# Optimization experiments

Measured on AMD Instinct MI355X. Metric: run time of the kernel, lower is better.

Reference implementation:

```python
import jax, jax.numpy as jnp
import numpy as np

CONNECTIONS = {0: [1, 7], 1: [0, 2], 2: [1, 3], 3: [2], 4: [0, 5], 5: [4, 6], 6: [5], 7: [0, 8], 8: [7, 9, 11, 14], 9: [8, 10], 10: [9], 11: [8, 12], 12: [11, 13], 13: [12], 14: [8, 15], 15: [14, 16], 16: [15]}
J = 17
DIM_IN = 128
DIM_OUT = 128
B, T = 64, 243


def _build_bases():
    A1 = np.zeros((J, J), dtype=np.float32)
    for i, neigh in CONNECTIONS.items():
        for j in neigh:
            A1[i, j] = 1.0
            A1[j, i] = 1.0
    eye = np.eye(J, dtype=np.float32)
    adj1_base = A1 + eye
    paths2 = (A1 @ A1 > 0).astype(np.float32)
    adj2_base = ((paths2 - A1 - eye) > 0).astype(np.float32)
    return jnp.asarray(adj1_base), jnp.asarray(adj2_base)


def setup_inputs() -> dict:
    key = jax.random.key(0)
    ks = jax.random.split(key, 8)
    adj1_base, adj2_base = _build_bases()
    # xavier_uniform with gain 1.414 for W
    bound_w = 1.414 * np.sqrt(6.0 / (DIM_IN + DIM_OUT))
    W = jax.random.uniform(ks[0], (DIM_IN, DIM_OUT), jnp.float32, -bound_w, bound_w)
    bound_b = 1.0 / np.sqrt(DIM_IN)
    b = jax.random.uniform(ks[1], (DIM_OUT,), jnp.float32, -bound_b, bound_b)
    return {
        "x": jax.random.normal(ks[2], (B, T, J, DIM_IN), jnp.float32),
        "W": W,
        "b": b,
        "adj_l1": jnp.zeros((J, J), jnp.float32),
        "adj_l2": jnp.zeros((J, J), jnp.float32),
        "w1": jnp.ones((1,), jnp.float32),
        "w2": jnp.ones((1,), jnp.float32),
        "gate_w": jax.random.normal(ks[3], (DIM_IN, 1), jnp.float32) / np.sqrt(DIM_IN),
        "gate_b": jnp.zeros((1,), jnp.float32),
        "bn_gamma": jnp.ones((DIM_OUT,), jnp.float32),
        "bn_beta": jnp.zeros((DIM_OUT,), jnp.float32),
        "adj1_base": adj1_base,
        "adj2_base": adj2_base,
    }


def reference(x, W, b, adj_l1, adj_l2, w1, w2, gate_w, gate_b, bn_gamma, bn_beta, adj1_base, adj2_base):
    Bb, Tt, Jj, C = x.shape
    xf = x.reshape(Bb * Tt, Jj, C)  # (N, J, C)

    # learnable-weighted static adjacency (symmetrized)
    A1w = adj1_base + jax.nn.sigmoid(adj_l1)
    A2w = adj2_base + jax.nn.sigmoid(adj_l2)
    comb = jax.nn.softplus(w1[0]) * A1w + jax.nn.softplus(w2[0]) * A2w
    comb = 0.5 * (comb + comb.T)  # (J, J)

    # dynamic cosine-similarity adjacency
    nrm = jnp.linalg.norm(xf, axis=-1, keepdims=True)
    xn = xf / jnp.maximum(nrm, 1e-12)
    dyn = jax.nn.relu(jnp.einsum("nic,njc->nij", xn, xn)) + jnp.eye(Jj, dtype=x.dtype)

    gate = jax.nn.sigmoid(xf @ gate_w + gate_b)  # (N, J, 1)
    A = gate * comb[None] + (1.0 - gate) * dyn  # (N, J, J)

    # symmetric degree normalization
    deg = A.sum(-1)  # (N, J)
    d = (deg + 1e-6) ** -0.5
    A_hat = d[:, :, None] * A * d[:, None, :]

    h = jnp.einsum("nij,njc->nic", A_hat, xf @ W) + b  # (N, J, dim_out)

    # BatchNorm1d over channels (training-mode batch stats over N and J)
    mean = h.mean(axis=(0, 1))
    var = h.var(axis=(0, 1))
    h = (h - mean) * jax.lax.rsqrt(var + 1e-5) * bn_gamma + bn_beta

    h = jax.nn.relu(h)
    h = h + xf  # residual (dim_in == dim_out -> identity projection)
    return h.reshape(Bb, Tt, Jj, -1)
```

## Files before the change

kernel.cpp:

```cpp
#include <hip/hip_runtime.h>

typedef unsigned short u16;
typedef unsigned int   u32;
typedef __attribute__((ext_vector_type(8))) short bfrag8;
typedef __attribute__((ext_vector_type(4))) float f32x4;

#define NSAMP  15552
#define GRID_B 3888
#define GRID_G 4131

__device__ __forceinline__ u32 bfr(float f){
  u32 u = __float_as_uint(f);
  return (u + 0x7FFFu + ((u >> 16) & 1u)) >> 16;
}
__device__ __forceinline__ u32 packbf(float lo, float hi){
  return bfr(lo) | (bfr(hi) << 16);
}
__device__ __forceinline__ float sigm(float v){ return 1.0f / (1.0f + __expf(-v)); }
__device__ __forceinline__ float softp(float v){ return (v > 20.f) ? v : log1pf(__expf(v)); }

__global__ void kA(const float* __restrict__ W, const float* __restrict__ al1,
                   const float* __restrict__ al2, const float* __restrict__ w1,
                   const float* __restrict__ w2, const float* __restrict__ a1b,
                   const float* __restrict__ a2b, u16* __restrict__ wt,
                   float* __restrict__ comb, float* __restrict__ mid){
  int idx = blockIdx.x * 256 + threadIdx.x;
  int k = idx >> 7, n = idx & 127;
  wt[n * 128 + k] = (u16)bfr(W[idx]);
  if (blockIdx.x == 1) mid[threadIdx.x] = 0.f;
  if (blockIdx.x == 0){
    float s1 = softp(w1[0]);
    float s2 = softp(w2[0]);
    for (int p = threadIdx.x; p < 289; p += 256){
      int i = p / 17, j = p - i * 17;
      float mij = s1 * (a1b[i*17+j] + sigm(al1[i*17+j])) + s2 * (a2b[i*17+j] + sigm(al2[i*17+j]));
      float mji = s1 * (a1b[j*17+i] + sigm(al1[j*17+i])) + s2 * (a2b[j*17+i] + sigm(al2[j*17+i]));
      comb[i*20 + j] = 0.5f * (mij + mji);
    }
  }
}

struct __align__(16) QSmem { u16 xb[4][18][136]; };
__global__ __launch_bounds__(256, 4) void kQ(const float* __restrict__ x,
    const float* __restrict__ gw, const float* __restrict__ gb,
    float* __restrict__ gbuf){
  __shared__ QSmem q;
  const int tid = threadIdx.x;
  const int w  = tid >> 6;
  const int l  = tid & 63;
  const int g4 = l >> 4;
  const int lc = l & 15;
  const int s  = blockIdx.x * 4 + w;
  const float* xs = x + (size_t)s * 2176;

  float2 g2 = *(const float2*)(gw + 2*l);
  *(u32*)&q.xb[w][17][2*l] = packbf(g2.x, g2.y);
  #pragma unroll
  for (int j = 0; j < 17; j++){
    float2 v = *(const float2*)(xs + j*128 + 2*l);
    *(u32*)&q.xb[w][j][2*l] = packbf(v.x, v.y);
  }
  __syncthreads();
  __builtin_amdgcn_sched_barrier(0);

  const int rB = 16 + ((lc < 2) ? lc : 1);
  f32x4 z4 = {0.f,0.f,0.f,0.f};
  f32x4 dg00 = z4, dg01 = z4, dg11 = z4;
  #pragma unroll
  for (int ks = 0; ks < 4; ks++){
    const int ko = ks*32 + (g4 << 3);
    bfrag8 a0 = *(const bfrag8*)&q.xb[w][lc][ko];
    bfrag8 a1 = *(const bfrag8*)&q.xb[w][rB][ko];
    dg00 = __builtin_amdgcn_mfma_f32_16x16x32_bf16(a0, a0, dg00, 0,0,0);
    dg01 = __builtin_amdgcn_mfma_f32_16x16x32_bf16(a0, a1, dg01, 0,0,0);
    dg11 = __builtin_amdgcn_mfma_f32_16x16x32_bf16(a1, a1, dg11, 0,0,0);
  }
  float* gs = gbuf + (size_t)s * 384;
  const float gbv = gb[0];
  #pragma unroll
  for (int r = 0; r < 4; r++){
    const int i = (g4 << 2) + r;
    gs[i*20 + lc] = dg00[r];
    if (lc == 0){ gs[i*20 + 16] = dg01[r]; gs[16*20 + i] = dg01[r]; }
    if (lc == 1){ gs[360 + i] = sigm(dg01[r] + gbv); }
  }
  if ((lc >> 2) == g4){
    float v = dg00[lc & 3];
    gs[340 + lc] = 1.0f / fmaxf(sqrtf(v), 1e-12f);
  }
  if (l == 0) gs[340 + 16] = 1.0f / fmaxf(sqrtf(dg11[0]), 1e-12f);
  if (l == 1) gs[360 + 16] = sigm(dg11[0] + gbv);
}

struct WaveMem {
  float G[17][20];
  float scr[64];
};
struct BSmem {
  WaveMem wm[4];
  float   combs[340];
};
static_assert(sizeof(BSmem) <= 81920, "LDS budget");

__global__ __launch_bounds__(256, 4) void kBl(
    const float* __restrict__ x, const float* __restrict__ combg,
    const float* __restrict__ gbuf, float* __restrict__ out){
  __shared__ BSmem sm;
  const int tid = threadIdx.x;
  const int w  = tid >> 6;
  const int l  = tid & 63;
  const int g4 = l >> 4;
  const int lc = l & 15;

  for (int p = tid; p < 340; p += 256) sm.combs[p] = combg[p];

  WaveMem& M = sm.wm[w];
  float* Mf = (float*)&M.G[0][0];
  const int s = blockIdx.x * 4 + w;
  const float* gs = gbuf + (size_t)s * 384;
  for (int p = l; p < 380; p += 64) Mf[p] = gs[p];

  const float* xs = x + (size_t)s * 2176;
  float2 xr[17];
  #pragma unroll
  for (int j = 0; j < 17; j++) xr[j] = *(const float2*)(xs + j*128 + 2*l);
  __syncthreads();

  const float iv16 = M.scr[16], gt16 = M.scr[36];
  const float ivj  = M.scr[lc];
  float av00[4], av01[4], dp0[4];
  #pragma unroll
  for (int r = 0; r < 4; r++){
    const int i0 = (g4 << 2) + r;
    const float iv0 = M.scr[i0], gi0 = M.scr[20 + i0];
    float dyn = (i0 == lc) ? 2.0f : fmaxf(M.G[i0][lc] * iv0 * ivj, 0.f);
    av00[r] = gi0 * sm.combs[i0*20 + lc] + (1.f - gi0) * dyn;
    float dyn16 = fmaxf(M.G[i0][16] * iv0 * iv16, 0.f);
    float a16 = gi0 * sm.combs[i0*20 + 16] + (1.f - gi0) * dyn16;
    av01[r] = (lc == 0) ? a16 : 0.f;
    dp0[r] = av00[r] + av01[r];
  }
  float dyn10 = fmaxf(M.G[16][lc] * iv16 * ivj, 0.f);
  float av10 = gt16 * sm.combs[16*20 + lc] + (1.f - gt16) * dyn10;
  float av11 = (lc == 0) ? (gt16 * sm.combs[16*20 + 16] + (1.f - gt16) * 2.0f) : 0.f;
  float dp1 = av10 + av11;
  #pragma unroll
  for (int m = 1; m <= 8; m <<= 1){
    #pragma unroll
    for (int r = 0; r < 4; r++) dp0[r] += __shfl_xor(dp0[r], m, 64);
    dp1 += __shfl_xor(dp1, m, 64);
  }
  float dd0[4];
  #pragma unroll
  for (int r = 0; r < 4; r++) dd0[r] = rsqrtf(dp0[r] + 1e-6f);
  float dd1 = rsqrtf(dp1 + 1e-6f);
  if (lc == 0){
    #pragma unroll
    for (int r = 0; r < 4; r++) M.scr[40 + (g4<<2) + r] = dd0[r];
  }
  if (l == 0) M.scr[40 + 16] = dd1;
  __syncthreads();

  const float dj0 = M.scr[40 + lc];
  const float dj1 = M.scr[40 + 16];
  #pragma unroll
  for (int r = 0; r < 4; r++){
    const int i0 = (g4 << 2) + r;
    M.G[i0][lc] = dd0[r] * av00[r] * dj0;
    if (lc == 0) M.G[i0][16] = dd0[r] * av01[r] * dj1;
  }
  if (g4 == 0) M.G[16][lc] = dd1 * av10 * dj0;
  if (l == 0)  M.G[16][16] = dd1 * av11 * dj1;
  __syncthreads();

  float* ob = out + (size_t)s * 2176;
  for (int i = 0; i < 17; i++){
    const float4 a0 = *(const float4*)&M.G[i][0];
    const float4 a1 = *(const float4*)&M.G[i][4];
    const float4 a2 = *(const float4*)&M.G[i][8];
    const float4 a3 = *(const float4*)&M.G[i][12];
    const float a16 = M.G[i][16];
    float zx = a0.x*xr[0].x,  zy = a0.x*xr[0].y;
    zx += a0.y*xr[1].x;  zy += a0.y*xr[1].y;
    zx += a0.z*xr[2].x;  zy += a0.z*xr[2].y;
    zx += a0.w*xr[3].x;  zy += a0.w*xr[3].y;
    zx += a1.x*xr[4].x;  zy += a1.x*xr[4].y;
    zx += a1.y*xr[5].x;  zy += a1.y*xr[5].y;
    zx += a1.z*xr[6].x;  zy += a1.z*xr[6].y;
    zx += a1.w*xr[7].x;  zy += a1.w*xr[7].y;
    zx += a2.x*xr[8].x;  zy += a2.x*xr[8].y;
    zx += a2.y*xr[9].x;  zy += a2.y*xr[9].y;
    zx += a2.z*xr[10].x; zy += a2.z*xr[10].y;
    zx += a2.w*xr[11].x; zy += a2.w*xr[11].y;
    zx += a3.x*xr[12].x; zy += a3.x*xr[12].y;
    zx += a3.y*xr[13].x; zy += a3.y*xr[13].y;
    zx += a3.z*xr[14].x; zy += a3.z*xr[14].y;
    zx += a3.w*xr[15].x; zy += a3.w*xr[15].y;
    zx += a16*xr[16].x;  zy += a16*xr[16].y;
    float2 zv; zv.x = zx; zv.y = zy;
    *(float2*)&ob[i*128 + 2*l] = zv;
  }
}

__global__ __launch_bounds__(256, 4) void kBf(
    const float* __restrict__ x, const float* __restrict__ gw,
    const float* __restrict__ gb, const float* __restrict__ combg,
    float* __restrict__ out){
  __shared__ BSmem sm;
  const int tid = threadIdx.x;
  const int w  = tid >> 6;
  const int l  = tid & 63;
  const int g4 = l >> 4;
  const int lc = l & 15;

  for (int p = tid; p < 340; p += 256) sm.combs[p] = combg[p];
  __syncthreads();

  WaveMem& M = sm.wm[w];
  float2 g2 = *(const float2*)(gw + 2*l);
  const float gbv = gb[0];
  const int s = blockIdx.x * 4 + w;
  const float* xs = x + (size_t)s * 2176;
  float2 xr[17];
  #pragma unroll
  for (int j = 0; j < 17; j++) xr[j] = *(const float2*)(xs + j*128 + 2*l);

  #pragma unroll
  for (int i = 0; i < 17; i++){
    float p[17];
    #pragma unroll
    for (int j = i; j < 17; j++)
      p[j-i] = xr[i].x*xr[j].x + xr[i].y*xr[j].y;
    float pg = xr[i].x*g2.x + xr[i].y*g2.y;
    #pragma unroll
    for (int m = 1; m <= 32; m <<= 1){
      #pragma unroll
      for (int j = i; j < 17; j++) p[j-i] += __shfl_xor(p[j-i], m, 64);
      pg += __shfl_xor(pg, m, 64);
    }
    #pragma unroll
    for (int j = i; j < 17; j++){
      if (l == j) M.G[i][j] = p[j-i];
      if (i != j && l == i) M.G[j][i] = p[j-i];
    }
    if (l == i){
      M.scr[i]      = 1.0f / fmaxf(sqrtf(p[0]), 1e-12f);
      M.scr[20 + i] = sigm(pg + gbv);
    }
  }
  __syncthreads();

  const float iv16 = M.scr[16], gt16 = M.scr[36];
  const float ivj  = M.scr[lc];
  float av00[4], av01[4], dp0[4];
  #pragma unroll
  for (int r = 0; r < 4; r++){
    const int i0 = (g4 << 2) + r;
    const float iv0 = M.scr[i0], gi0 = M.scr[20 + i0];
    float dyn = (i0 == lc) ? 2.0f : fmaxf(M.G[i0][lc] * iv0 * ivj, 0.f);
    av00[r] = gi0 * sm.combs[i0*20 + lc] + (1.f - gi0) * dyn;
    float dyn16 = fmaxf(M.G[i0][16] * iv0 * iv16, 0.f);
    float a16 = gi0 * sm.combs[i0*20 + 16] + (1.f - gi0) * dyn16;
    av01[r] = (lc == 0) ? a16 : 0.f;
    dp0[r] = av00[r] + av01[r];
  }
  float dyn10 = fmaxf(M.G[16][lc] * iv16 * ivj, 0.f);
  float av10 = gt16 * sm.combs[16*20 + lc] + (1.f - gt16) * dyn10;
  float av11 = (lc == 0) ? (gt16 * sm.combs[16*20 + 16] + (1.f - gt16) * 2.0f) : 0.f;
  float dp1 = av10 + av11;
  #pragma unroll
  for (int m = 1; m <= 8; m <<= 1){
    #pragma unroll
    for (int r = 0; r < 4; r++) dp0[r] += __shfl_xor(dp0[r], m, 64);
    dp1 += __shfl_xor(dp1, m, 64);
  }
  float dd0[4];
  #pragma unroll
  for (int r = 0; r < 4; r++) dd0[r] = rsqrtf(dp0[r] + 1e-6f);
  float dd1 = rsqrtf(dp1 + 1e-6f);
  if (lc == 0){
    #pragma unroll
    for (int r = 0; r < 4; r++) M.scr[40 + (g4<<2) + r] = dd0[r];
  }
  if (l == 0) M.scr[40 + 16] = dd1;
  __syncthreads();

  const float dj0 = M.scr[40 + lc];
  const float dj1 = M.scr[40 + 16];
  #pragma unroll
  for (int r = 0; r < 4; r++){
    const int i0 = (g4 << 2) + r;
    M.G[i0][lc] = dd0[r] * av00[r] * dj0;
    if (lc == 0) M.G[i0][16] = dd0[r] * av01[r] * dj1;
  }
  if (g4 == 0) M.G[16][lc] = dd1 * av10 * dj0;
  if (l == 0)  M.G[16][16] = dd1 * av11 * dj1;
  __syncthreads();

  float* ob = out + (size_t)s * 2176;
  for (int i = 0; i < 17; i++){
    const float4 a0 = *(const float4*)&M.G[i][0];
    const float4 a1 = *(const float4*)&M.G[i][4];
    const float4 a2 = *(const float4*)&M.G[i][8];
    const float4 a3 = *(const float4*)&M.G[i][12];
    const float a16 = M.G[i][16];
    float zx = a0.x*xr[0].x,  zy = a0.x*xr[0].y;
    zx += a0.y*xr[1].x;  zy += a0.y*xr[1].y;
    zx += a0.z*xr[2].x;  zy += a0.z*xr[2].y;
    zx += a0.w*xr[3].x;  zy += a0.w*xr[3].y;
    zx += a1.x*xr[4].x;  zy += a1.x*xr[4].y;
    zx += a1.y*xr[5].x;  zy += a1.y*xr[5].y;
    zx += a1.z*xr[6].x;  zy += a1.z*xr[6].y;
    zx += a1.w*xr[7].x;  zy += a1.w*xr[7].y;
    zx += a2.x*xr[8].x;  zy += a2.x*xr[8].y;
    zx += a2.y*xr[9].x;  zy += a2.y*xr[9].y;
    zx += a2.z*xr[10].x; zy += a2.z*xr[10].y;
    zx += a2.w*xr[11].x; zy += a2.w*xr[11].y;
    zx += a3.x*xr[12].x; zy += a3.x*xr[12].y;
    zx += a3.y*xr[13].x; zy += a3.y*xr[13].y;
    zx += a3.z*xr[14].x; zy += a3.z*xr[14].y;
    zx += a3.w*xr[15].x; zy += a3.w*xr[15].y;
    zx += a16*xr[16].x;  zy += a16*xr[16].y;
    float2 zv; zv.x = zx; zv.y = zy;
    *(float2*)&ob[i*128 + 2*l] = zv;
  }
}

struct __align__(16) GSmem {
  u16 wl[128][132];
  u16 zl[4][16][132];
};
__global__ __launch_bounds__(256, 3) void kG(const u16* __restrict__ wtg,
    float* __restrict__ mid, float* __restrict__ out){
  __shared__ GSmem g;
  const int tid = threadIdx.x;
  const int w  = tid >> 6;
  const int l  = tid & 63;
  const int g4 = l >> 4;
  const int lc = l & 15;

  for (int p = tid; p < 8192; p += 256){
    int n = p >> 6, k2 = (p & 63) * 2;
    *(u32*)&g.wl[n][k2] = ((const u32*)wtg)[p];
  }
  const int R = blockIdx.x * 64 + w * 16;
  float* zg = out + (size_t)R * 128;
  #pragma unroll
  for (int r = 0; r < 16; r++){
    float2 zv = *(const float2*)&zg[r*128 + 2*l];
    *(u32*)&g.zl[w][r][2*l] = packbf(zv.x, zv.y);
  }
  __syncthreads();
  __builtin_amdgcn_sched_barrier(0);

  f32x4 zero4 = {0.f,0.f,0.f,0.f};
  f32x4 acc[8];
  #pragma unroll
  for (int nf = 0; nf < 8; nf++) acc[nf] = zero4;
  #pragma unroll
  for (int ks = 0; ks < 4; ks++){
    const int ko = ks*32 + (g4 << 3);
    bfrag8 za = *(const bfrag8*)&g.zl[w][lc][ko];
    #pragma unroll
    for (int nf = 0; nf < 8; nf++){
      bfrag8 bw = *(const bfrag8*)&g.wl[nf*16 + lc][ko];
      acc[nf] = __builtin_amdgcn_mfma_f32_16x16x32_bf16(za, bw, acc[nf], 0,0,0);
    }
  }

  float s[8], q[8];
  #pragma unroll
  for (int nf = 0; nf < 8; nf++){
    float ss = 0.f, qq = 0.f;
    #pragma unroll
    for (int r = 0; r < 4; r++){
      float v = acc[nf][r];
      zg[(4*g4 + r)*128 + nf*16 + lc] = v;
      ss += v; qq += v*v;
    }
    ss += __shfl_xor(ss, 16, 64); ss += __shfl_xor(ss, 32, 64);
    qq += __shfl_xor(qq, 16, 64); qq += __shfl_xor(qq, 32, 64);
    s[nf] = ss; q[nf] = qq;
  }

  __syncthreads();
  float* stash = (float*)&g.zl[w][0][0];
  if (l < 16){
    #pragma unroll
    for (int nf = 0; nf < 8; nf++){
      stash[nf*16 + l]       = s[nf];
      stash[128 + nf*16 + l] = q[nf];
    }
  }
  __syncthreads();
  float t0 = ((float*)&g.zl[0][0][0])[tid];
  float t1 = ((float*)&g.zl[1][0][0])[tid];
  float t2 = ((float*)&g.zl[2][0][0])[tid];
  float t3 = ((float*)&g.zl[3][0][0])[tid];
  atomicAdd(&mid[tid], t0 + t1 + t2 + t3);
}

__global__ __launch_bounds__(256) void kD(const float* __restrict__ x,
    const float* __restrict__ mid, const float* __restrict__ gamma,
    const float* __restrict__ beta, float* __restrict__ out){
  __shared__ float sc[128], sh[128];
  const int t = threadIdx.x;
  if (t < 128){
    const float ic = 1.0f / 264384.0f;
    float mean = mid[t] * ic;
    float var  = fmaxf(mid[128 + t] * ic - mean*mean, 0.f);
    float scl  = gamma[t] * rsqrtf(var + 1e-5f);
    sc[t] = scl;
    sh[t] = beta[t] - mean * scl;
  }
  __syncthreads();
  const int total = 8460288;
  for (int i = blockIdx.x*256 + t; i < total; i += 2048*256){
    float4 h  = ((const float4*)out)[i];
    float4 xv = ((const float4*)x)[i];
    int c0 = (i & 31) << 2;
    float4 r;
    r.x = fmaxf(h.x*sc[c0+0] + sh[c0+0], 0.f) + xv.x;
    r.y = fmaxf(h.y*sc[c0+1] + sh[c0+1], 0.f) + xv.y;
    r.z = fmaxf(h.z*sc[c0+2] + sh[c0+2], 0.f) + xv.z;
    r.w = fmaxf(h.w*sc[c0+3] + sh[c0+3], 0.f) + xv.w;
    ((float4*)out)[i] = r;
  }
}

extern "C" void kernel_launch(void* const* d_in, const int* in_sizes, int n_in,
                              void* d_out, int out_size, void* d_ws, size_t ws_size,
                              hipStream_t stream){
  (void)in_sizes; (void)n_in; (void)out_size;
  const float* x     = (const float*)d_in[0];
  const float* W     = (const float*)d_in[1];
  const float* al1   = (const float*)d_in[3];
  const float* al2   = (const float*)d_in[4];
  const float* w1    = (const float*)d_in[5];
  const float* w2    = (const float*)d_in[6];
  const float* gw    = (const float*)d_in[7];
  const float* gb    = (const float*)d_in[8];
  const float* gamma = (const float*)d_in[9];
  const float* beta  = (const float*)d_in[10];
  const float* a1b   = (const float*)d_in[11];
  const float* a2b   = (const float*)d_in[12];
  float* out = (float*)d_out;

  float* wsf  = (float*)d_ws;
  float* comb = wsf;
  u16*   wt   = (u16*)(wsf + 384);
  float* mid  = wsf + 384 + 8192;
  float* gbuf = wsf + 384 + 8192 + 256;
  const size_t need = (size_t)(384 + 8192 + 256 + (size_t)NSAMP*384) * 4;

  hipLaunchKernelGGL(kA, dim3(64), dim3(256), 0, stream, W, al1, al2, w1, w2, a1b, a2b, wt, comb, mid);
  if (ws_size >= need){
    hipLaunchKernelGGL(kQ,  dim3(GRID_B), dim3(256), 0, stream, x, gw, gb, gbuf);
    hipLaunchKernelGGL(kBl, dim3(GRID_B), dim3(256), 0, stream, x, comb, gbuf, out);
  } else {
    hipLaunchKernelGGL(kBf, dim3(GRID_B), dim3(256), 0, stream, x, gw, gb, comb, out);
  }
  hipLaunchKernelGGL(kG, dim3(GRID_G), dim3(256), 0, stream, wt, mid, out);
  hipLaunchKernelGGL(kD, dim3(2048),   dim3(256), 0, stream, x, mid, gamma, beta, out);
}
```

Measured before the change: 256.3 us.

## Write aggregated features as bf16 to workspace and feed GEMM directly from global

The aggregation kernel now writes its A_hat·x result as packed bf16 into a separate workspace buffer instead of fp32 into the output. A new GEMM kernel reads these bf16 rows and the transposed weights straight from global memory into MFMA fragments, without staging them in LDS. It then writes h and accumulates per-channel batch-norm sums with atomics. The aim is to halve the intermediate traffic and drop the LDS staging and fp32-to-bf16 conversion in the GEMM. In exchange it needs a larger workspace and does more uncoalesced global reads of the weights.

```diff
diff --git a/kernel.cpp b/kernel.cpp
--- a/kernel.cpp
+++ b/kernel.cpp
@@ -102,9 +102,11 @@
 };
 static_assert(sizeof(BSmem) <= 81920, "LDS budget");
 
-__global__ __launch_bounds__(256, 4) void kBl(
+template<int ZOUT>
+__device__ __forceinline__ void kBl_body(
     const float* __restrict__ x, const float* __restrict__ combg,
-    const float* __restrict__ gbuf, float* __restrict__ out){
+    const float* __restrict__ gbuf, float* __restrict__ out,
+    u16* __restrict__ zbuf){
   __shared__ BSmem sm;
   const int tid = threadIdx.x;
   const int w  = tid >> 6;
@@ -124,6 +126,146 @@
   float2 xr[17];
   #pragma unroll
   for (int j = 0; j < 17; j++) xr[j] = *(const float2*)(xs + j*128 + 2*l);
+  __syncthreads();
+
+  const float iv16 = M.scr[16], gt16 = M.scr[36];
+  const float ivj  = M.scr[lc];
+  float av00[4], av01[4], dp0[4];
+  #pragma unroll
+  for (int r = 0; r < 4; r++){
+    const int i0 = (g4 << 2) + r;
+    const float iv0 = M.scr[i0], gi0 = M.scr[20 + i0];
+    float dyn = (i0 == lc) ? 2.0f : fmaxf(M.G[i0][lc] * iv0 * ivj, 0.f);
+    av00[r] = gi0 * sm.combs[i0*20 + lc] + (1.f - gi0) * dyn;
+    float dyn16 = fmaxf(M.G[i0][16] * iv0 * iv16, 0.f);
+    float a16 = gi0 * sm.combs[i0*20 + 16] + (1.f - gi0) * dyn16;
+    av01[r] = (lc == 0) ? a16 : 0.f;
+    dp0[r] = av00[r] + av01[r];
+  }
+  float dyn10 = fmaxf(M.G[16][lc] * iv16 * ivj, 0.f);
+  float av10 = gt16 * sm.combs[16*20 + lc] + (1.f - gt16) * dyn10;
+  float av11 = (lc == 0) ? (gt16 * sm.combs[16*20 + 16] + (1.f - gt16) * 2.0f) : 0.f;
+  float dp1 = av10 + av11;
+  #pragma unroll
+  for (int m = 1; m <= 8; m <<= 1){
+    #pragma unroll
+    for (int r = 0; r < 4; r++) dp0[r] += __shfl_xor(dp0[r], m, 64);
+    dp1 += __shfl_xor(dp1, m, 64);
+  }
+  float dd0[4];
+  #pragma unroll
+  for (int r = 0; r < 4; r++) dd0[r] = rsqrtf(dp0[r] + 1e-6f);
+  float dd1 = rsqrtf(dp1 + 1e-6f);
+  if (lc == 0){
+    #pragma unroll
+    for (int r = 0; r < 4; r++) M.scr[40 + (g4<<2) + r] = dd0[r];
+  }
+  if (l == 0) M.scr[40 + 16] = dd1;
+  __syncthreads();
+
+  const float dj0 = M.scr[40 + lc];
+  const float dj1 = M.scr[40 + 16];
+  #pragma unroll
+  for (int r = 0; r < 4; r++){
+    const int i0 = (g4 << 2) + r;
+    M.G[i0][lc] = dd0[r] * av00[r] * dj0;
+    if (lc == 0) M.G[i0][16] = dd0[r] * av01[r] * dj1;
+  }
+  if (g4 == 0) M.G[16][lc] = dd1 * av10 * dj0;
+  if (l == 0)  M.G[16][16] = dd1 * av11 * dj1;
+  __syncthreads();
+
+  float* ob = out + (size_t)s * 2176;
+  u16*   zb = zbuf + (size_t)s * 2176;
+  for (int i = 0; i < 17; i++){
+    const float4 a0 = *(const float4*)&M.G[i][0];
+    const float4 a1 = *(const float4*)&M.G[i][4];
+    const float4 a2 = *(const float4*)&M.G[i][8];
+    const float4 a3 = *(const float4*)&M.G[i][12];
+    const float a16 = M.G[i][16];
+    float zx = a0.x*xr[0].x,  zy = a0.x*xr[0].y;
+    zx += a0.y*xr[1].x;  zy += a0.y*xr[1].y;
+    zx += a0.z*xr[2].x;  zy += a0.z*xr[2].y;
+    zx += a0.w*xr[3].x;  zy += a0.w*xr[3].y;
+    zx += a1.x*xr[4].x;  zy += a1.x*xr[4].y;
+    zx += a1.y*xr[5].x;  zy += a1.y*xr[5].y;
+    zx += a1.z*xr[6].x;  zy += a1.z*xr[6].y;
+    zx += a1.w*xr[7].x;  zy += a1.w*xr[7].y;
+    zx += a2.x*xr[8].x;  zy += a2.x*xr[8].y;
+    zx += a2.y*xr[9].x;  zy += a2.y*xr[9].y;
+    zx += a2.z*xr[10].x; zy += a2.z*xr[10].y;
+    zx += a2.w*xr[11].x; zy += a2.w*xr[11].y;
+    zx += a3.x*xr[12].x; zy += a3.x*xr[12].y;
+    zx += a3.y*xr[13].x; zy += a3.y*xr[13].y;
+    zx += a3.z*xr[14].x; zy += a3.z*xr[14].y;
+    zx += a3.w*xr[15].x; zy += a3.w*xr[15].y;
+    zx += a16*xr[16].x;  zy += a16*xr[16].y;
+    if (ZOUT == 1){
+      *(u32*)&zb[i*128 + 2*l] = packbf(zx, zy);
+    } else {
+      float2 zv; zv.x = zx; zv.y = zy;
+      *(float2*)&ob[i*128 + 2*l] = zv;
+    }
+  }
+}
+
+__global__ __launch_bounds__(256, 4) void kBl2(
+    const float* __restrict__ x, const float* __restrict__ combg,
+    const float* __restrict__ gbuf, u16* __restrict__ zbuf){
+  kBl_body<1>(x, combg, gbuf, nullptr, zbuf);
+}
+__global__ __launch_bounds__(256, 4) void kBl(
+    const float* __restrict__ x, const float* __restrict__ combg,
+    const float* __restrict__ gbuf, float* __restrict__ out){
+  kBl_body<0>(x, combg, gbuf, out, nullptr);
+}
+
+__global__ __launch_bounds__(256, 4) void kBf(
+    const float* __restrict__ x, const float* __restrict__ gw,
+    const float* __restrict__ gb, const float* __restrict__ combg,
+    float* __restrict__ out){
+  __shared__ BSmem sm;
+  const int tid = threadIdx.x;
+  const int w  = tid >> 6;
+  const int l  = tid & 63;
+  const int g4 = l >> 4;
+  const int lc = l & 15;
+
+  for (int p = tid; p < 340; p += 256) sm.combs[p] = combg[p];
+  __syncthreads();
+
+  WaveMem& M = sm.wm[w];
+  float2 g2 = *(const float2*)(gw + 2*l);
+  const float gbv = gb[0];
+  const int s = blockIdx.x * 4 + w;
+  const float* xs = x + (size_t)s * 2176;
+  float2 xr[17];
+  #pragma unroll
+  for (int j = 0; j < 17; j++) xr[j] = *(const float2*)(xs + j*128 + 2*l);
+
+  #pragma unroll
+  for (int i = 0; i < 17; i++){
+    float p[17];
+    #pragma unroll
+    for (int j = i; j < 17; j++)
+      p[j-i] = xr[i].x*xr[j].x + xr[i].y*xr[j].y;
+    float pg = xr[i].x*g2.x + xr[i].y*g2.y;
+    #pragma unroll
+    for (int m = 1; m <= 32; m <<= 1){
+      #pragma unroll
+      for (int j = i; j < 17; j++) p[j-i] += __shfl_xor(p[j-i], m, 64);
+      pg += __shfl_xor(pg, m, 64);
+    }
+    #pragma unroll
+    for (int j = i; j < 17; j++){
+      if (l == j) M.G[i][j] = p[j-i];
+      if (i != j && l == i) M.G[j][i] = p[j-i];
+    }
+    if (l == i){
+      M.scr[i]      = 1.0f / fmaxf(sqrtf(p[0]), 1e-12f);
+      M.scr[20 + i] = sigm(pg + gbv);
+    }
+  }
   __syncthreads();
 
   const float iv16 = M.scr[16], gt16 = M.scr[36];
@@ -202,128 +344,57 @@
   }
 }
 
-__global__ __launch_bounds__(256, 4) void kBf(
-    const float* __restrict__ x, const float* __restrict__ gw,
-    const float* __restrict__ gb, const float* __restrict__ combg,
+__global__ __launch_bounds__(256, 4) void kG2(const u16* __restrict__ wtg,
+    const u16* __restrict__ zbuf, float* __restrict__ mid,
     float* __restrict__ out){
-  __shared__ BSmem sm;
+  __shared__ float stash[4][256];
   const int tid = threadIdx.x;
   const int w  = tid >> 6;
   const int l  = tid & 63;
   const int g4 = l >> 4;
   const int lc = l & 15;
-
-  for (int p = tid; p < 340; p += 256) sm.combs[p] = combg[p];
-  __syncthreads();
-
-  WaveMem& M = sm.wm[w];
-  float2 g2 = *(const float2*)(gw + 2*l);
-  const float gbv = gb[0];
-  const int s = blockIdx.x * 4 + w;
-  const float* xs = x + (size_t)s * 2176;
-  float2 xr[17];
-  #pragma unroll
-  for (int j = 0; j < 17; j++) xr[j] = *(const float2*)(xs + j*128 + 2*l);
-
-  #pragma unroll
-  for (int i = 0; i < 17; i++){
-    float p[17];
-    #pragma unroll
-    for (int j = i; j < 17; j++)
-      p[j-i] = xr[i].x*xr[j].x + xr[i].y*xr[j].y;
-    float pg = xr[i].x*g2.x + xr[i].y*g2.y;
-    #pragma unroll
-    for (int m = 1; m <= 32; m <<= 1){
-      #pragma unroll
-      for (int j = i; j < 17; j++) p[j-i] += __shfl_xor(p[j-i], m, 64);
-      pg += __shfl_xor(pg, m, 64);
-    }
-    #pragma unroll
-    for (int j = i; j < 17; j++){
-      if (l == j) M.G[i][j] = p[j-i];
-      if (i != j && l == i) M.G[j][i] = p[j-i];
-    }
-    if (l == i){
-      M.scr[i]      = 1.0f / fmaxf(sqrtf(p[0]), 1e-12f);
-      M.scr[20 + i] = sigm(pg + gbv);
-    }
-  }
-  __syncthreads();
-
-  const float iv16 = M.scr[16], gt16 = M.scr[36];
-  const float ivj  = M.scr[lc];
-  float av00[4], av01[4], dp0[4];
-  #pragma unroll
-  for (int r = 0; r < 4; r++){
-    const int i0 = (g4 << 2) + r;
-    const float iv0 = M.scr[i0], gi0 = M.scr[20 + i0];
-    float dyn = (i0 == lc) ? 2.0f : fmaxf(M.G[i0][lc] * iv0 * ivj, 0.f);
-    av00[r] = gi0 * sm.combs[i0*20 + lc] + (1.f - gi0) * dyn;
-    float dyn16 = fmaxf(M.G[i0][16] * iv0 * iv16, 0.f);
-    float a16 = gi0 * sm.combs[i0*20 + 16] + (1.f - gi0) * dyn16;
-    av01[r] = (lc == 0) ? a16 : 0.f;
-    dp0[r] = av00[r] + av01[r];
-  }
-  float dyn10 = fmaxf(M.G[16][lc] * iv16 * ivj, 0.f);
-  float av10 = gt16 * sm.combs[16*20 + lc] + (1.f - gt16) * dyn10;
-  float av11 = (lc == 0) ? (gt16 * sm.combs[16*20 + 16] + (1.f - gt16) * 2.0f) : 0.f;
-  float dp1 = av10 + av11;
-  #pragma unroll
-  for (int m = 1; m <= 8; m <<= 1){
-    #pragma unroll
-    for (int r = 0; r < 4; r++) dp0[r] += __shfl_xor(dp0[r], m, 64);
-    dp1 += __shfl_xor(dp1, m, 64);
-  }
-  float dd0[4];
-  #pragma unroll
-  for (int r = 0; r < 4; r++) dd0[r] = rsqrtf(dp0[r] + 1e-6f);
-  float dd1 = rsqrtf(dp1 + 1e-6f);
-  if (lc == 0){
-    #pragma unroll
-    for (int r = 0; r < 4; r++) M.scr[40 + (g4<<2) + r] = dd0[r];
-  }
-  if (l == 0) M.scr[40 + 16] = dd1;
-  __syncthreads();
-
-  const float dj0 = M.scr[40 + lc];
-  const float dj1 = M.scr[40 + 16];
-  #pragma unroll
-  for (int r = 0; r < 4; r++){
-    const int i0 = (g4 << 2) + r;
-    M.G[i0][lc] = dd0[r] * av00[r] * dj0;
-    if (lc == 0) M.G[i0][16] = dd0[r] * av01[r] * dj1;
-  }
-  if (g4 == 0) M.G[16][lc] = dd1 * av10 * dj0;
-  if (l == 0)  M.G[16][16] = dd1 * av11 * dj1;
-  __syncthreads();
-
-  float* ob = out + (size_t)s * 2176;
-  for (int i = 0; i < 17; i++){
-    const float4 a0 = *(const float4*)&M.G[i][0];
-    const float4 a1 = *(const float4*)&M.G[i][4];
-    const float4 a2 = *(const float4*)&M.G[i][8];
-    const float4 a3 = *(const float4*)&M.G[i][12];
-    const float a16 = M.G[i][16];
-    float zx = a0.x*xr[0].x,  zy = a0.x*xr[0].y;
-    zx += a0.y*xr[1].x;  zy += a0.y*xr[1].y;
-    zx += a0.z*xr[2].x;  zy += a0.z*xr[2].y;
-    zx += a0.w*xr[3].x;  zy += a0.w*xr[3].y;
-    zx += a1.x*xr[4].x;  zy += a1.x*xr[4].y;
-    zx += a1.y*xr[5].x;  zy += a1.y*xr[5].y;
-    zx += a1.z*xr[6].x;  zy += a1.z*xr[6].y;
-    zx += a1.w*xr[7].x;  zy += a1.w*xr[7].y;
-    zx += a2.x*xr[8].x;  zy += a2.x*xr[8].y;
-    zx += a2.y*xr[9].x;  zy += a2.y*xr[9].y;
-    zx += a2.z*xr[10].x; zy += a2.z*xr[10].y;
-    zx += a2.w*xr[11].x; zy += a2.w*xr[11].y;
-    zx += a3.x*xr[12].x; zy += a3.x*xr[12].y;
-    zx += a3.y*xr[13].x; zy += a3.y*xr[13].y;
-    zx += a3.z*xr[14].x; zy += a3.z*xr[14].y;
-    zx += a3.w*xr[15].x; zy += a3.w*xr[15].y;
-    zx += a16*xr[16].x;  zy += a16*xr[16].y;
-    float2 zv; zv.x = zx; zv.y = zy;
-    *(float2*)&ob[i*128 + 2*l] = zv;
-  }
+  const int R = blockIdx.x * 64 + w * 16;
+
+  const u16* zr = zbuf + (size_t)R * 128;
+  f32x4 zero4 = {0.f,0.f,0.f,0.f};
+  f32x4 acc[8];
+  #pragma unroll
+  for (int nf = 0; nf < 8; nf++) acc[nf] = zero4;
+  #pragma unroll
+  for (int ks = 0; ks < 4; ks++){
+    const int ko = ks*32 + (g4 << 3);
+    bfrag8 za = *(const bfrag8*)&zr[lc * 128 + ko];
+    #pragma unroll
+    for (int nf = 0; nf < 8; nf++){
+      bfrag8 bw = *(const bfrag8*)&wtg[(nf*16 + lc)*128 + ko];
+      acc[nf] = __builtin_amdgcn_mfma_f32_16x16x32_bf16(za, bw, acc[nf], 0,0,0);
+    }
+  }
+
+  float* hg = out + (size_t)R * 128;
+  float s[8], q[8];
+  #pragma unroll
+  for (int nf = 0; nf < 8; nf++){
+    float ss = 0.f, qq = 0.f;
+    #pragma unroll
+    for (int r = 0; r < 4; r++){
+      float v = acc[nf][r];
+      hg[(4*g4 + r)*128 + nf*16 + lc] = v;
+      ss += v; qq += v*v;
+    }
+    ss += __shfl_xor(ss, 16, 64); ss += __shfl_xor(ss, 32, 64);
+    qq += __shfl_xor(qq, 16, 64); qq += __shfl_xor(qq, 32, 64);
+    s[nf] = ss; q[nf] = qq;
+  }
+  if (l < 16){
+    #pragma unroll
+    for (int nf = 0; nf < 8; nf++){
+      stash[w][nf*16 + l]       = s[nf];
+      stash[w][128 + nf*16 + l] = q[nf];
+    }
+  }
+  __syncthreads();
+  atomicAdd(&mid[tid], stash[0][tid] + stash[1][tid] + stash[2][tid] + stash[3][tid]);
 }
 
 struct __align__(16) GSmem {
@@ -451,15 +522,23 @@
   u16*   wt   = (u16*)(wsf + 384);
   float* mid  = wsf + 384 + 8192;
   float* gbuf = wsf + 384 + 8192 + 256;
-  const size_t need = (size_t)(384 + 8192 + 256 + (size_t)NSAMP*384) * 4;
+  u16*   zbuf = (u16*)(gbuf + (size_t)NSAMP*384);
+  const size_t base  = (size_t)(384 + 8192 + 256) * 4;
+  const size_t need1 = base + (size_t)NSAMP*384*4;
+  const size_t need2 = need1 + (size_t)NSAMP*2176*2;
 
   hipLaunchKernelGGL(kA, dim3(64), dim3(256), 0, stream, W, al1, al2, w1, w2, a1b, a2b, wt, comb, mid);
-  if (ws_size >= need){
+  if (ws_size >= need2){
+    hipLaunchKernelGGL(kQ,   dim3(GRID_B), dim3(256), 0, stream, x, gw, gb, gbuf);
+    hipLaunchKernelGGL(kBl2, dim3(GRID_B), dim3(256), 0, stream, x, comb, gbuf, zbuf);
+    hipLaunchKernelGGL(kG2,  dim3(GRID_G), dim3(256), 0, stream, wt, zbuf, mid, out);
+  } else if (ws_size >= need1){
     hipLaunchKernelGGL(kQ,  dim3(GRID_B), dim3(256), 0, stream, x, gw, gb, gbuf);
     hipLaunchKernelGGL(kBl, dim3(GRID_B), dim3(256), 0, stream, x, comb, gbuf, out);
+    hipLaunchKernelGGL(kG,  dim3(GRID_G), dim3(256), 0, stream, wt, mid, out);
   } else {
     hipLaunchKernelGGL(kBf, dim3(GRID_B), dim3(256), 0, stream, x, gw, gb, comb, out);
-  }
-  hipLaunchKernelGGL(kG, dim3(GRID_G), dim3(256), 0, stream, wt, mid, out);
-  hipLaunchKernelGGL(kD, dim3(2048),   dim3(256), 0, stream, x, mid, gamma, beta, out);
-}
+    hipLaunchKernelGGL(kG,  dim3(GRID_G), dim3(256), 0, stream, wt, mid, out);
+  }
+  hipLaunchKernelGGL(kD, dim3(2048), dim3(256), 0, stream, x, mid, gamma, beta, out);
+}
```

Result: slower. 266.0 us (+3.8%).
